# Kernel tuning notes

Measured on AMD Instinct MI355X. Metric: run time of the kernel, lower is better.

The kernel has to match this reference:

```python
import jax, jax.numpy as jnp
import numpy as np

H = 16  # num_heads


def setup_inputs() -> dict:
    key = jax.random.key(0)
    ks = jax.random.split(key, 8)
    B, T, D = 2, 2048, 1024
    hd = D // H
    s = 0.02
    return {
        "x": jax.random.normal(ks[0], (B, T, D), jnp.float32),
        "position_bias": jax.random.normal(ks[1], (H, T, T), jnp.float32) * 0.1,
        "Wq": jax.random.normal(ks[2], (D, D), jnp.float32) * s,
        "bq": jnp.zeros((D,), jnp.float32),
        "Wk": jax.random.normal(ks[3], (D, D), jnp.float32) * s,
        "bk": jnp.zeros((D,), jnp.float32),
        "Wv": jax.random.normal(ks[4], (D, D), jnp.float32) * s,
        "bv": jnp.zeros((D,), jnp.float32),
        "Wo": jax.random.normal(ks[5], (D, D), jnp.float32) * s,
        "bo": jnp.zeros((D,), jnp.float32),
        "Wg": jax.random.normal(ks[6], (8, hd), jnp.float32) * s,
        "bg": jnp.zeros((8,), jnp.float32),
        "gru_const": jnp.ones((1, H, 1, 1), jnp.float32),
    }


def reference(x, position_bias, Wq, bq, Wk, bk, Wv, bv, Wo, bo, Wg, bg, gru_const):
    B, T, D = x.shape
    hd = D // H
    # gated relative position bias
    gated_input = x.reshape(B, T, H, hd).transpose(0, 2, 1, 3)  # (B,H,T,hd)
    rp = jnp.einsum('bhtd,ed->bhte', gated_input, Wg) + bg       # (B,H,T,8)
    rp = rp.reshape(B, H, T, 2, 4).sum(-1)                        # (B,H,T,2)
    rp = jax.nn.sigmoid(rp)
    gate_a, gate_b = rp[..., 0:1], rp[..., 1:2]                   # (B,H,T,1)
    gate_input = gate_a * (gate_b * gru_const - 1.0) + 2.0        # (B,H,T,1)
    gated_bias = gate_input * position_bias                       # (B,H,T,T)
    # scaled dot-product attention
    q = (x @ Wq.T + bq).reshape(B, T, H, hd).transpose(0, 2, 1, 3)
    k = (x @ Wk.T + bk).reshape(B, T, H, hd).transpose(0, 2, 1, 3)
    v = (x @ Wv.T + bv).reshape(B, T, H, hd).transpose(0, 2, 1, 3)
    scale = 1.0 / jnp.sqrt(jnp.asarray(hd, x.dtype))
    scores = jnp.einsum('bhqd,bhkd->bhqk', q, k) * scale + gated_bias
    attn = jax.nn.softmax(scores, axis=-1)
    out = jnp.einsum('bhqk,bhkd->bhqd', attn, v)                  # (B,H,T,hd)
    out = out.transpose(0, 2, 1, 3).reshape(B, T, D)
    return out @ Wo.T + bo
```

## Files before the change

### kernel.cpp

```cpp
#include <hip/hip_runtime.h>
#include <stdint.h>

typedef unsigned short u16;
typedef __attribute__((ext_vector_type(8))) short short8;
typedef __attribute__((ext_vector_type(4))) float f32x4;

__device__ __forceinline__ u16 f2bf(float f) {
  union { float f; uint32_t u; } v; v.f = f;
  uint32_t r = (v.u + 0x7fffu + ((v.u >> 16) & 1u)) >> 16;
  return (u16)r;
}

__device__ __forceinline__ f32x4 mfma16(short8 a, short8 b, f32x4 c) {
  return __builtin_amdgcn_mfma_f32_16x16x32_bf16(a, b, c, 0, 0, 0);
}

typedef __attribute__((address_space(3))) void lds_void;
typedef __attribute__((address_space(1))) void glb_void;
__device__ __forceinline__ void gld_lds16(const void* gp, void* lp) {
  __builtin_amdgcn_global_load_lds((const glb_void*)gp, (lds_void*)lp, 16, 0, 0);
}

__global__ __launch_bounds__(256) void cvt_bf16(const float* __restrict__ in,
                                                u16* __restrict__ out, int n4) {
  int i = blockIdx.x * 256 + threadIdx.x;
  if (i >= n4) return;
  const float4 v = ((const float4*)in)[i];
  ushort4 o;
  o.x = f2bf(v.x); o.y = f2bf(v.y); o.z = f2bf(v.z); o.w = f2bf(v.w);
  ((ushort4*)out)[i] = o;
}

__global__ __launch_bounds__(256) void gates_kernel(
    const float* __restrict__ x, const float* __restrict__ Wg,
    const float* __restrict__ bg, const float* __restrict__ gru,
    float* __restrict__ gates) {
  __shared__ float wga[64], wgb[64], bsum[2];
  int tid = threadIdx.x;
  if (tid < 64) {
    float a = 0.f, b = 0.f;
#pragma unroll
    for (int e = 0; e < 4; ++e) a += Wg[e * 64 + tid];
#pragma unroll
    for (int e = 4; e < 8; ++e) b += Wg[e * 64 + tid];
    wga[tid] = a; wgb[tid] = b;
  }
  if (tid == 0) bsum[0] = bg[0] + bg[1] + bg[2] + bg[3];
  if (tid == 1) bsum[1] = bg[4] + bg[5] + bg[6] + bg[7];
  __syncthreads();
  int l16 = tid & 15;
  int row = blockIdx.x * 16 + (tid >> 4);
  int b = row >> 15, h = (row >> 11) & 15, t = row & 2047;
  const float4 xv = *(const float4*)&x[(b * 2048 + t) * 1024 + h * 64 + l16 * 4];
  float pa = xv.x * wga[l16 * 4] + xv.y * wga[l16 * 4 + 1] +
             xv.z * wga[l16 * 4 + 2] + xv.w * wga[l16 * 4 + 3];
  float pq = xv.x * wgb[l16 * 4] + xv.y * wgb[l16 * 4 + 1] +
             xv.z * wgb[l16 * 4 + 2] + xv.w * wgb[l16 * 4 + 3];
#pragma unroll
  for (int off = 1; off < 16; off <<= 1) {
    pa += __shfl_xor(pa, off);
    pq += __shfl_xor(pq, off);
  }
  if (l16 == 0) {
    float ga = 1.f / (1.f + __expf(-(pa + bsum[0])));
    float gb = 1.f / (1.f + __expf(-(pq + bsum[1])));
    gates[row] = ga * (gb * gru[h] - 1.0f) + 2.0f;
  }
}

__global__ __launch_bounds__(256) void gemm_bt(
    const u16* __restrict__ A,
    const u16* __restrict__ W0, const u16* __restrict__ W1, const u16* __restrict__ W2,
    const float* __restrict__ c0, const float* __restrict__ c1, const float* __restrict__ c2,
    void* d0, void* d1, void* d2, int fbase) {
  __shared__ __align__(16) u16 As[128 * 32];
  __shared__ __align__(16) u16 Bs[128 * 32];
  const int z = blockIdx.z;
  const int f = fbase + z;
  const u16* W = (z == 0) ? W0 : (z == 1 ? W1 : W2);
  const float* bias = (z == 0) ? c0 : (z == 1 ? c1 : c2);
  void* dst = (z == 0) ? d0 : (z == 1 ? d1 : d2);

  const int m0 = blockIdx.x * 128, n0 = blockIdx.y * 128;
  const int tid = threadIdx.x;
  const int w = tid >> 6, lane = tid & 63, l16 = lane & 15, quad = lane >> 4;
  const int wm = w >> 1, wn = w & 1;

  f32x4 acc[4][4] = {};

  for (int kt = 0; kt < 32; ++kt) {
    const int k0 = kt * 32;
    __syncthreads();
#pragma unroll
    for (int j = 0; j < 2; ++j) {
      int c = tid + j * 256;
      int row = c >> 2, dc = c & 3;
      gld_lds16(&A[(m0 + row) * 1024 + k0 + dc * 8], &As[c * 8]);
      gld_lds16(&W[(n0 + row) * 1024 + k0 + dc * 8], &Bs[c * 8]);
    }
    __syncthreads();
    short8 af[4], bf[4];
#pragma unroll
    for (int i = 0; i < 4; ++i) {
      af[i] = *(const short8*)&As[(wm * 64 + i * 16 + l16) * 32 + quad * 8];
      bf[i] = *(const short8*)&Bs[(wn * 64 + i * 16 + l16) * 32 + quad * 8];
    }
#pragma unroll
    for (int mb = 0; mb < 4; ++mb)
#pragma unroll
      for (int nb = 0; nb < 4; ++nb)
        acc[mb][nb] = mfma16(af[mb], bf[nb], acc[mb][nb]);
  }

  if (f < 3) {
    u16* out = (u16*)dst;
#pragma unroll
    for (int nb = 0; nb < 4; ++nb) {
      int gn = n0 + wn * 64 + nb * 16 + l16;
      float bv = bias[gn];
      int hh = gn >> 6, dd = gn & 63;
#pragma unroll
      for (int mb = 0; mb < 4; ++mb)
#pragma unroll
        for (int r = 0; r < 4; ++r) {
          int gm = m0 + wm * 64 + mb * 16 + quad * 4 + r;
          int bb = gm >> 11, t = gm & 2047;
          out[((bb * 16 + hh) * 2048 + t) * 64 + dd] = f2bf(acc[mb][nb][r] + bv);
        }
    }
  } else {
    float* out = (float*)dst;
#pragma unroll
    for (int nb = 0; nb < 4; ++nb) {
      int gn = n0 + wn * 64 + nb * 16 + l16;
      float bv = bias[gn];
#pragma unroll
      for (int mb = 0; mb < 4; ++mb)
#pragma unroll
        for (int r = 0; r < 4; ++r) {
          int gm = m0 + wm * 64 + mb * 16 + quad * 4 + r;
          out[gm * 1024 + gn] = acc[mb][nb][r] + bv;
        }
    }
  }
}

__global__ __launch_bounds__(256) void vtrans(const u16* __restrict__ v,
                                              u16* __restrict__ vt) {
  __shared__ __align__(16) u16 lds[64 * 72];
  const int bh = blockIdx.y, t0 = blockIdx.x * 64;
  const int tid = threadIdx.x;
#pragma unroll
  for (int j = 0; j < 2; ++j) {
    int c = tid + j * 256;
    int tr = c >> 3, dc = c & 7;
    union { int4 v4; u16 u[8]; } uu;
    uu.v4 = *(const int4*)&v[(bh * 2048 + t0 + tr) * 64 + dc * 8];
#pragma unroll
    for (int jj = 0; jj < 8; ++jj) lds[(dc * 8 + jj) * 72 + tr] = uu.u[jj];
  }
  __syncthreads();
#pragma unroll
  for (int j = 0; j < 2; ++j) {
    int c = tid + j * 256;
    int dr = c >> 3, tc = c & 7;
    int4 vv = *(const int4*)&lds[dr * 72 + tc * 8];
    *(int4*)&vt[(bh * 64 + dr) * 2048 + t0 + tc * 8] = vv;
  }
}

__global__ __launch_bounds__(256) void attn_kernel(
    const u16* __restrict__ q, const u16* __restrict__ k,
    const u16* __restrict__ vt, const float* __restrict__ pb,
    const float* __restrict__ gates, u16* __restrict__ ao) {
  __shared__ __align__(16) u16 Ks[2][64 * 72];
  __shared__ __align__(16) u16 Vs[2][64 * 72];
  __shared__ __align__(16) u16 Ps[4][16 * 72];

  const int qt = blockIdx.x, h = blockIdx.y;
  const int tid = threadIdx.x, w = tid >> 6, lane = tid & 63;
  const int l16 = lane & 15, quad = lane >> 4;
  const int m0 = qt * 64 + w * 16;

  short8 Qa[2][2];
  float g8[2][4];
#pragma unroll
  for (int b = 0; b < 2; ++b) {
    const u16* qp = &q[((b * 16 + h) * 2048 + m0 + l16) * 64];
    Qa[b][0] = *(const short8*)&qp[quad * 8];
    Qa[b][1] = *(const short8*)&qp[32 + quad * 8];
#pragma unroll
    for (int r = 0; r < 4; ++r)
      g8[b][r] = gates[(b * 16 + h) * 2048 + m0 + quad * 4 + r] * 8.0f;
  }

  f32x4 O[2][4] = {};
  float mi[2][4], li[2][4];
#pragma unroll
  for (int b = 0; b < 2; ++b)
#pragma unroll
    for (int r = 0; r < 4; ++r) { mi[b][r] = -3.0e38f; li[b][r] = 0.f; }

  for (int kt = 0; kt < 32; ++kt) {
    const int k0 = kt * 64;
    float pbv[4][4];
#pragma unroll
    for (int nb = 0; nb < 4; ++nb)
#pragma unroll
      for (int r = 0; r < 4; ++r)
        pbv[nb][r] = pb[(h * 2048 + m0 + quad * 4 + r) * 2048 + k0 + nb * 16 + l16];

    __syncthreads();
#pragma unroll
    for (int j = 0; j < 4; ++j) {
      int c = tid + j * 256;
      int bb = c >> 9, row = (c >> 3) & 63, ch = c & 7;
      int4 kv = *(const int4*)&k[((bb * 16 + h) * 2048 + k0 + row) * 64 + ch * 8];
      *(int4*)&Ks[bb][row * 72 + ch * 8] = kv;
      int4 vv = *(const int4*)&vt[((bb * 16 + h) * 64 + row) * 2048 + k0 + ch * 8];
      *(int4*)&Vs[bb][row * 72 + ch * 8] = vv;
    }
    __syncthreads();

#pragma unroll
    for (int b = 0; b < 2; ++b) {
      f32x4 acc[4];
#pragma unroll
      for (int nb = 0; nb < 4; ++nb) {
        short8 kf0 = *(const short8*)&Ks[b][(nb * 16 + l16) * 72 + quad * 8];
        short8 kf1 = *(const short8*)&Ks[b][(nb * 16 + l16) * 72 + 32 + quad * 8];
        f32x4 z = {};
        z = mfma16(Qa[b][0], kf0, z);
        acc[nb] = mfma16(Qa[b][1], kf1, z);
      }
      float Sv[4][4], rm[4];
#pragma unroll
      for (int nb = 0; nb < 4; ++nb)
#pragma unroll
        for (int r = 0; r < 4; ++r)
          Sv[nb][r] = (acc[nb][r] + g8[b][r] * pbv[nb][r]) * 0.125f;
#pragma unroll
      for (int r = 0; r < 4; ++r)
        rm[r] = fmaxf(fmaxf(Sv[0][r], Sv[1][r]), fmaxf(Sv[2][r], Sv[3][r]));
#pragma unroll
      for (int off = 1; off < 16; off <<= 1)
#pragma unroll
        for (int r = 0; r < 4; ++r)
          rm[r] = fmaxf(rm[r], __shfl_xor(rm[r], off));
      float al[4], rs[4];
#pragma unroll
      for (int r = 0; r < 4; ++r) {
        float mn = fmaxf(mi[b][r], rm[r]);
        al[r] = __expf(mi[b][r] - mn);
        mi[b][r] = mn;
        rs[r] = 0.f;
      }
#pragma unroll
      for (int nb = 0; nb < 4; ++nb)
#pragma unroll
        for (int r = 0; r < 4; ++r) {
          float p = __expf(Sv[nb][r] - mi[b][r]);
          Sv[nb][r] = p;
          rs[r] += p;
        }
#pragma unroll
      for (int off = 1; off < 16; off <<= 1)
#pragma unroll
        for (int r = 0; r < 4; ++r)
          rs[r] += __shfl_xor(rs[r], off);
#pragma unroll
      for (int r = 0; r < 4; ++r)
        li[b][r] = li[b][r] * al[r] + rs[r];
#pragma unroll
      for (int hb = 0; hb < 4; ++hb)
#pragma unroll
        for (int r = 0; r < 4; ++r)
          O[b][hb][r] *= al[r];
#pragma unroll
      for (int nb = 0; nb < 4; ++nb)
#pragma unroll
        for (int r = 0; r < 4; ++r)
          Ps[w][(quad * 4 + r) * 72 + nb * 16 + l16] = f2bf(Sv[nb][r]);
      __asm__ volatile("s_waitcnt lgkmcnt(0)" ::: "memory");
      short8 pa0 = *(const short8*)&Ps[w][l16 * 72 + quad * 8];
      short8 pa1 = *(const short8*)&Ps[w][l16 * 72 + 32 + quad * 8];
#pragma unroll
      for (int hb = 0; hb < 4; ++hb) {
        short8 vf0 = *(const short8*)&Vs[b][(hb * 16 + l16) * 72 + quad * 8];
        short8 vf1 = *(const short8*)&Vs[b][(hb * 16 + l16) * 72 + 32 + quad * 8];
        O[b][hb] = mfma16(pa0, vf0, O[b][hb]);
        O[b][hb] = mfma16(pa1, vf1, O[b][hb]);
      }
    }
  }
#pragma unroll
  for (int b = 0; b < 2; ++b) {
    float inv[4];
#pragma unroll
    for (int r = 0; r < 4; ++r) inv[r] = 1.0f / li[b][r];
#pragma unroll
    for (int hb = 0; hb < 4; ++hb)
#pragma unroll
      for (int r = 0; r < 4; ++r) {
        int t = m0 + quad * 4 + r;
        int col = h * 64 + hb * 16 + l16;
        ao[(b * 2048 + t) * 1024 + col] = f2bf(O[b][hb][r] * inv[r]);
      }
  }
}

extern "C" void kernel_launch(void* const* d_in, const int* in_sizes, int n_in,
                              void* d_out, int out_size, void* d_ws, size_t ws_size,
                              hipStream_t stream) {
  const float* x   = (const float*)d_in[0];
  const float* pb  = (const float*)d_in[1];
  const float* Wq  = (const float*)d_in[2];
  const float* bq  = (const float*)d_in[3];
  const float* Wk  = (const float*)d_in[4];
  const float* bk  = (const float*)d_in[5];
  const float* Wv  = (const float*)d_in[6];
  const float* bv  = (const float*)d_in[7];
  const float* Wo  = (const float*)d_in[8];
  const float* bo  = (const float*)d_in[9];
  const float* Wg  = (const float*)d_in[10];
  const float* bg  = (const float*)d_in[11];
  const float* gru = (const float*)d_in[12];
  float* out = (float*)d_out;

  char* ws = (char*)d_ws;
  u16*   xb   = (u16*)(ws);
  u16*   wqb  = (u16*)(ws + (8u  << 20));
  u16*   wkb  = (u16*)(ws + (10u << 20));
  u16*   wvb  = (u16*)(ws + (12u << 20));
  u16*   wob  = (u16*)(ws + (14u << 20));
  u16*   qws  = (u16*)(ws + (16u << 20));
  u16*   kws  = (u16*)(ws + (24u << 20));
  u16*   vws  = (u16*)(ws + (32u << 20));
  u16*   vtws = (u16*)(ws + (40u << 20));
  float* gws  = (float*)(ws + (48u << 20));
  u16*   aows = (u16*)(ws + (49u << 20));

  cvt_bf16<<<4096, 256, 0, stream>>>(x,  xb,  1048576);
  cvt_bf16<<<1024, 256, 0, stream>>>(Wq, wqb, 262144);
  cvt_bf16<<<1024, 256, 0, stream>>>(Wk, wkb, 262144);
  cvt_bf16<<<1024, 256, 0, stream>>>(Wv, wvb, 262144);
  cvt_bf16<<<1024, 256, 0, stream>>>(Wo, wob, 262144);
  gates_kernel<<<4096, 256, 0, stream>>>(x, Wg, bg, gru, gws);
  gemm_bt<<<dim3(32, 8, 3), 256, 0, stream>>>(xb, wqb, wkb, wvb, bq, bk, bv,
                                              qws, kws, vws, 0);
  vtrans<<<dim3(32, 32), 256, 0, stream>>>(vws, vtws);
  attn_kernel<<<dim3(32, 16), 256, 0, stream>>>(qws, kws, vtws, pb, gws, aows);
  gemm_bt<<<dim3(32, 8, 1), 256, 0, stream>>>(aows, wob, wob, wob, bo, bo, bo,
                                              out, out, out, 3);
}
```

Baseline: 556.4 us.

## Fuse conversion kernels, double-buffer attention tiles, drop online softmax max tracking

Merges the five bf16 conversion launches and the gates kernel into one launch that reads x once. In the attention kernel, K/V tiles are double-buffered through direct global-to-LDS loads with an XOR swizzle in place of padding, and the position bias for the next tile is prefetched. The online-softmax running max and rescaling are removed, so the kernel exponentiates raw scores and reduces the row sum once at the end. That saves per-tile shuffles and rescales but risks overflow if scores grow large.

After: 511.0 us. 8.2% less time.

```diff
diff --git a/kernel.cpp b/kernel.cpp
--- a/kernel.cpp
+++ b/kernel.cpp
@@ -21,22 +21,26 @@
   __builtin_amdgcn_global_load_lds((const glb_void*)gp, (lds_void*)lp, 16, 0, 0);
 }
 
-__global__ __launch_bounds__(256) void cvt_bf16(const float* __restrict__ in,
-                                                u16* __restrict__ out, int n4) {
-  int i = blockIdx.x * 256 + threadIdx.x;
-  if (i >= n4) return;
-  const float4 v = ((const float4*)in)[i];
-  ushort4 o;
-  o.x = f2bf(v.x); o.y = f2bf(v.y); o.z = f2bf(v.z); o.w = f2bf(v.w);
-  ((ushort4*)out)[i] = o;
-}
-
-__global__ __launch_bounds__(256) void gates_kernel(
+__global__ __launch_bounds__(256) void cvt_gates(
     const float* __restrict__ x, const float* __restrict__ Wg,
     const float* __restrict__ bg, const float* __restrict__ gru,
-    float* __restrict__ gates) {
+    const float* __restrict__ wq, const float* __restrict__ wk,
+    const float* __restrict__ wv, const float* __restrict__ wo,
+    u16* __restrict__ xb, float* __restrict__ gates, u16* __restrict__ wqb,
+    u16* __restrict__ wkb, u16* __restrict__ wvb, u16* __restrict__ wob) {
+  const int bid = blockIdx.x, tid = threadIdx.x;
+  if (bid >= 4096) {
+    int s = (bid - 4096) >> 10, r = (bid - 4096) & 1023;
+    const float* src = (s == 0) ? wq : (s == 1) ? wk : (s == 2) ? wv : wo;
+    u16* dst = (s == 0) ? wqb : (s == 1) ? wkb : (s == 2) ? wvb : wob;
+    int i = r * 256 + tid;
+    const float4 v = ((const float4*)src)[i];
+    ushort4 o;
+    o.x = f2bf(v.x); o.y = f2bf(v.y); o.z = f2bf(v.z); o.w = f2bf(v.w);
+    ((ushort4*)dst)[i] = o;
+    return;
+  }
   __shared__ float wga[64], wgb[64], bsum[2];
-  int tid = threadIdx.x;
   if (tid < 64) {
     float a = 0.f, b = 0.f;
 #pragma unroll
@@ -48,23 +52,26 @@
   if (tid == 0) bsum[0] = bg[0] + bg[1] + bg[2] + bg[3];
   if (tid == 1) bsum[1] = bg[4] + bg[5] + bg[6] + bg[7];
   __syncthreads();
-  int l16 = tid & 15;
-  int row = blockIdx.x * 16 + (tid >> 4);
-  int b = row >> 15, h = (row >> 11) & 15, t = row & 2047;
-  const float4 xv = *(const float4*)&x[(b * 2048 + t) * 1024 + h * 64 + l16 * 4];
-  float pa = xv.x * wga[l16 * 4] + xv.y * wga[l16 * 4 + 1] +
-             xv.z * wga[l16 * 4 + 2] + xv.w * wga[l16 * 4 + 3];
-  float pq = xv.x * wgb[l16 * 4] + xv.y * wgb[l16 * 4 + 1] +
-             xv.z * wgb[l16 * 4 + 2] + xv.w * wgb[l16 * 4 + 3];
+  const int i = bid * 256 + tid;
+  const float4 v = ((const float4*)x)[i];
+  ushort4 o;
+  o.x = f2bf(v.x); o.y = f2bf(v.y); o.z = f2bf(v.z); o.w = f2bf(v.w);
+  ((ushort4*)xb)[i] = o;
+  const int l16 = tid & 15;
+  float pa = v.x * wga[l16 * 4] + v.y * wga[l16 * 4 + 1] +
+             v.z * wga[l16 * 4 + 2] + v.w * wga[l16 * 4 + 3];
+  float pq = v.x * wgb[l16 * 4] + v.y * wgb[l16 * 4 + 1] +
+             v.z * wgb[l16 * 4 + 2] + v.w * wgb[l16 * 4 + 3];
 #pragma unroll
   for (int off = 1; off < 16; off <<= 1) {
     pa += __shfl_xor(pa, off);
     pq += __shfl_xor(pq, off);
   }
   if (l16 == 0) {
+    int h = tid >> 4, b = bid >> 11, t = bid & 2047;
     float ga = 1.f / (1.f + __expf(-(pa + bsum[0])));
     float gb = 1.f / (1.f + __expf(-(pq + bsum[1])));
-    gates[row] = ga * (gb * gru[h] - 1.0f) + 2.0f;
+    gates[(b * 16 + h) * 2048 + t] = ga * (gb * gru[h] - 1.0f) + 2.0f;
   }
 }
 
@@ -169,12 +176,12 @@
   }
 }
 
-__global__ __launch_bounds__(256) void attn_kernel(
+__global__ __launch_bounds__(256, 2) void attn_kernel(
     const u16* __restrict__ q, const u16* __restrict__ k,
     const u16* __restrict__ vt, const float* __restrict__ pb,
     const float* __restrict__ gates, u16* __restrict__ ao) {
-  __shared__ __align__(16) u16 Ks[2][64 * 72];
-  __shared__ __align__(16) u16 Vs[2][64 * 72];
+  __shared__ __align__(16) u16 Ks[2][2][4096];
+  __shared__ __align__(16) u16 Vs[2][2][4096];
   __shared__ __align__(16) u16 Ps[4][16 * 72];
 
   const int qt = blockIdx.x, h = blockIdx.y;
@@ -195,101 +202,80 @@
   }
 
   f32x4 O[2][4] = {};
-  float mi[2][4], li[2][4];
-#pragma unroll
-  for (int b = 0; b < 2; ++b)
-#pragma unroll
-    for (int r = 0; r < 4; ++r) { mi[b][r] = -3.0e38f; li[b][r] = 0.f; }
-
-  for (int kt = 0; kt < 32; ++kt) {
-    const int k0 = kt * 64;
-    float pbv[4][4];
-#pragma unroll
-    for (int nb = 0; nb < 4; ++nb)
-#pragma unroll
-      for (int r = 0; r < 4; ++r)
-        pbv[nb][r] = pb[(h * 2048 + m0 + quad * 4 + r) * 2048 + k0 + nb * 16 + l16];
-
-    __syncthreads();
-#pragma unroll
-    for (int j = 0; j < 4; ++j) {
-      int c = tid + j * 256;
-      int bb = c >> 9, row = (c >> 3) & 63, ch = c & 7;
-      int4 kv = *(const int4*)&k[((bb * 16 + h) * 2048 + k0 + row) * 64 + ch * 8];
-      *(int4*)&Ks[bb][row * 72 + ch * 8] = kv;
-      int4 vv = *(const int4*)&vt[((bb * 16 + h) * 64 + row) * 2048 + k0 + ch * 8];
-      *(int4*)&Vs[bb][row * 72 + ch * 8] = vv;
-    }
-    __syncthreads();
-
-#pragma unroll
-    for (int b = 0; b < 2; ++b) {
-      f32x4 acc[4];
-#pragma unroll
-      for (int nb = 0; nb < 4; ++nb) {
-        short8 kf0 = *(const short8*)&Ks[b][(nb * 16 + l16) * 72 + quad * 8];
-        short8 kf1 = *(const short8*)&Ks[b][(nb * 16 + l16) * 72 + 32 + quad * 8];
-        f32x4 z = {};
-        z = mfma16(Qa[b][0], kf0, z);
-        acc[nb] = mfma16(Qa[b][1], kf1, z);
+  float li[2][4] = {};
+
+#define STAGE(buf, kt)                                                          \
+  {                                                                             \
+    const int k0s = (kt) * 64;                                                  \
+    _Pragma("unroll") for (int j = 0; j < 4; ++j) {                             \
+      int c = tid + j * 256;                                                    \
+      int bb = c >> 9, row = (c >> 3) & 63, ch = c & 7;                         \
+      int gch = ch ^ (row & 7);                                                 \
+      gld_lds16(&k[((bb * 16 + h) * 2048 + k0s + row) * 64 + gch * 8],          \
+                &Ks[buf][bb][row * 64 + ch * 8]);                               \
+      gld_lds16(&vt[((bb * 16 + h) * 64 + row) * 2048 + k0s + gch * 8],         \
+                &Vs[buf][bb][row * 64 + ch * 8]);                               \
+    }                                                                           \
+  }
+
+  float pbv[2][4][4];
+  STAGE(0, 0);
+#pragma unroll
+  for (int nb = 0; nb < 4; ++nb)
+#pragma unroll
+    for (int r = 0; r < 4; ++r)
+      pbv[0][nb][r] = pb[(h * 2048 + m0 + quad * 4 + r) * 2048 + nb * 16 + l16];
+
+  for (int kt0 = 0; kt0 < 32; kt0 += 2) {
+#pragma unroll
+    for (int half = 0; half < 2; ++half) {
+      const int kt = kt0 + half;
+      const int p = half;
+      __syncthreads();
+      if (kt + 1 < 32) {
+        STAGE(1 - p, kt + 1);
+        const int k0n = (kt + 1) * 64;
+#pragma unroll
+        for (int nb = 0; nb < 4; ++nb)
+#pragma unroll
+          for (int r = 0; r < 4; ++r)
+            pbv[1 - p][nb][r] =
+                pb[(h * 2048 + m0 + quad * 4 + r) * 2048 + k0n + nb * 16 + l16];
       }
-      float Sv[4][4], rm[4];
-#pragma unroll
-      for (int nb = 0; nb < 4; ++nb)
-#pragma unroll
-        for (int r = 0; r < 4; ++r)
-          Sv[nb][r] = (acc[nb][r] + g8[b][r] * pbv[nb][r]) * 0.125f;
-#pragma unroll
-      for (int r = 0; r < 4; ++r)
-        rm[r] = fmaxf(fmaxf(Sv[0][r], Sv[1][r]), fmaxf(Sv[2][r], Sv[3][r]));
-#pragma unroll
-      for (int off = 1; off < 16; off <<= 1)
-#pragma unroll
-        for (int r = 0; r < 4; ++r)
-          rm[r] = fmaxf(rm[r], __shfl_xor(rm[r], off));
-      float al[4], rs[4];
-#pragma unroll
-      for (int r = 0; r < 4; ++r) {
-        float mn = fmaxf(mi[b][r], rm[r]);
-        al[r] = __expf(mi[b][r] - mn);
-        mi[b][r] = mn;
-        rs[r] = 0.f;
-      }
-#pragma unroll
-      for (int nb = 0; nb < 4; ++nb)
-#pragma unroll
-        for (int r = 0; r < 4; ++r) {
-          float p = __expf(Sv[nb][r] - mi[b][r]);
-          Sv[nb][r] = p;
-          rs[r] += p;
+#pragma unroll
+      for (int b = 0; b < 2; ++b) {
+        f32x4 acc[4];
+#pragma unroll
+        for (int nb = 0; nb < 4; ++nb) {
+          int row = nb * 16 + l16;
+          const u16* Kb = &Ks[p][b][row * 64];
+          short8 kf0 = *(const short8*)&Kb[(quad ^ (row & 7)) * 8];
+          short8 kf1 = *(const short8*)&Kb[((4 + quad) ^ (row & 7)) * 8];
+          f32x4 z = {};
+          z = mfma16(Qa[b][0], kf0, z);
+          acc[nb] = mfma16(Qa[b][1], kf1, z);
         }
 #pragma unroll
-      for (int off = 1; off < 16; off <<= 1)
-#pragma unroll
-        for (int r = 0; r < 4; ++r)
-          rs[r] += __shfl_xor(rs[r], off);
-#pragma unroll
-      for (int r = 0; r < 4; ++r)
-        li[b][r] = li[b][r] * al[r] + rs[r];
-#pragma unroll
-      for (int hb = 0; hb < 4; ++hb)
-#pragma unroll
-        for (int r = 0; r < 4; ++r)
-          O[b][hb][r] *= al[r];
-#pragma unroll
-      for (int nb = 0; nb < 4; ++nb)
-#pragma unroll
-        for (int r = 0; r < 4; ++r)
-          Ps[w][(quad * 4 + r) * 72 + nb * 16 + l16] = f2bf(Sv[nb][r]);
-      __asm__ volatile("s_waitcnt lgkmcnt(0)" ::: "memory");
-      short8 pa0 = *(const short8*)&Ps[w][l16 * 72 + quad * 8];
-      short8 pa1 = *(const short8*)&Ps[w][l16 * 72 + 32 + quad * 8];
-#pragma unroll
-      for (int hb = 0; hb < 4; ++hb) {
-        short8 vf0 = *(const short8*)&Vs[b][(hb * 16 + l16) * 72 + quad * 8];
-        short8 vf1 = *(const short8*)&Vs[b][(hb * 16 + l16) * 72 + 32 + quad * 8];
-        O[b][hb] = mfma16(pa0, vf0, O[b][hb]);
-        O[b][hb] = mfma16(pa1, vf1, O[b][hb]);
+        for (int nb = 0; nb < 4; ++nb)
+#pragma unroll
+          for (int r = 0; r < 4; ++r) {
+            float s = fmaf(g8[b][r], pbv[p][nb][r], acc[nb][r]) * 0.125f;
+            float e = __expf(s);
+            li[b][r] += e;
+            Ps[w][(quad * 4 + r) * 72 + nb * 16 + l16] = f2bf(e);
+          }
+        __asm__ volatile("s_waitcnt lgkmcnt(0)" ::: "memory");
+        short8 pa0 = *(const short8*)&Ps[w][l16 * 72 + quad * 8];
+        short8 pa1 = *(const short8*)&Ps[w][l16 * 72 + 32 + quad * 8];
+#pragma unroll
+        for (int hb = 0; hb < 4; ++hb) {
+          int row = hb * 16 + l16;
+          const u16* Vb = &Vs[p][b][row * 64];
+          short8 vf0 = *(const short8*)&Vb[(quad ^ (row & 7)) * 8];
+          short8 vf1 = *(const short8*)&Vb[((4 + quad) ^ (row & 7)) * 8];
+          O[b][hb] = mfma16(pa0, vf0, O[b][hb]);
+          O[b][hb] = mfma16(pa1, vf1, O[b][hb]);
+        }
       }
     }
   }
@@ -297,7 +283,12 @@
   for (int b = 0; b < 2; ++b) {
     float inv[4];
 #pragma unroll
-    for (int r = 0; r < 4; ++r) inv[r] = 1.0f / li[b][r];
+    for (int r = 0; r < 4; ++r) {
+      float s = li[b][r];
+#pragma unroll
+      for (int off = 1; off < 16; off <<= 1) s += __shfl_xor(s, off);
+      inv[r] = 1.0f / s;
+    }
 #pragma unroll
     for (int hb = 0; hb < 4; ++hb)
 #pragma unroll
@@ -340,12 +331,8 @@
   float* gws  = (float*)(ws + (48u << 20));
   u16*   aows = (u16*)(ws + (49u << 20));
 
-  cvt_bf16<<<4096, 256, 0, stream>>>(x,  xb,  1048576);
-  cvt_bf16<<<1024, 256, 0, stream>>>(Wq, wqb, 262144);
-  cvt_bf16<<<1024, 256, 0, stream>>>(Wk, wkb, 262144);
-  cvt_bf16<<<1024, 256, 0, stream>>>(Wv, wvb, 262144);
-  cvt_bf16<<<1024, 256, 0, stream>>>(Wo, wob, 262144);
-  gates_kernel<<<4096, 256, 0, stream>>>(x, Wg, bg, gru, gws);
+  cvt_gates<<<8192, 256, 0, stream>>>(x, Wg, bg, gru, Wq, Wk, Wv, Wo,
+                                      xb, gws, wqb, wkb, wvb, wob);
   gemm_bt<<<dim3(32, 8, 3), 256, 0, stream>>>(xb, wqb, wkb, wvb, bq, bk, bv,
                                               qws, kws, vws, 0);
   vtrans<<<dim3(32, 32), 256, 0, stream>>>(vws, vtws);
```
